# Performance work log

Hardware: AMD Instinct MI355X
Metric: run time of the kernel (lower is better)

The kernel has to match this reference:

```python
import jax, jax.numpy as jnp
from jax import lax
import numpy as np

MS = 128            # local_map_size
HALF = MS // 2
B, S = 8, 64
C, H, W = 3, 1024, 1024


def setup_inputs() -> dict:
    key = jax.random.key(0)
    ks = jax.random.split(key, 48)
    r = lambda i, shape, s: jax.random.normal(ks[i], shape, jnp.float32) * s
    z = lambda *shape: jnp.zeros(shape, jnp.float32)
    o = lambda *shape: jnp.ones(shape, jnp.float32)
    return {
        "full_map": jax.random.normal(ks[0], (B, C, H, W), jnp.float32),
        "conditions": jax.random.uniform(ks[1], (B, 5), jnp.float32, 0.0, 1024.0),
        "input_seq": jax.random.uniform(ks[2], (B, S, 2), jnp.float32, 0.0, 1024.0),
        "steps_remaining": jax.random.uniform(ks[3], (B, S), jnp.float32, 0.0, 500.0),
        # LocalMapEncoder convs (OIHW) + batchnorm affine params
        "cw1": r(4, (16, 3, 3, 3), 0.2),   "cb1": z(16),  "g1": o(16),  "be1": z(16),
        "cw2": r(5, (32, 16, 3, 3), 0.1),  "cb2": z(32),  "g2": o(32),  "be2": z(32),
        "cw3": r(6, (64, 32, 3, 3), 0.07), "cb3": z(64),  "g3": o(64),  "be3": z(64),
        "cw4": r(7, (128, 64, 3, 3), 0.05),"cb4": z(128), "g4": o(128), "be4": z(128),
        "fw1": r(8, (512, 128 * 8 * 8), 0.01), "fb1": z(512),
        "fw2": r(9, (256, 512), 0.04),         "fb2": z(256),
        # ConditionEncoder (6 -> 128 -> 64)
        "ew1": r(10, (128, 6), 0.05),  "eb1": z(128),
        "ew2": r(11, (64, 128), 0.05), "eb2": z(64),
        # coord embedder (2 -> 32)
        "mw": r(12, (32, 2), 0.05), "mb": z(32),
        # 2-layer LSTM, torch gate order (i, f, g, o)
        "w_ih0": r(13, (4 * 256, 32), 0.05),  "w_hh0": r(14, (4 * 256, 256), 0.05),
        "b_ih0": z(4 * 256), "b_hh0": z(4 * 256),
        "w_ih1": r(15, (4 * 256, 256), 0.05), "w_hh1": r(16, (4 * 256, 256), 0.05),
        "b_ih1": z(4 * 256), "b_hh1": z(4 * 256),
        # context layer (256+256+64=576 -> 128 -> 64) and output (64 -> 2)
        "xw1": r(17, (128, 576), 0.04), "xb1": z(128),
        "xw2": r(18, (64, 128), 0.05),  "xb2": z(64),
        "ow": r(19, (2, 64), 0.1),      "ob": z(2),
    }


def _conv_bn_relu(x, w, b, g, be):
    # stride-2 3x3 conv, padding 1, NCHW/OIHW; BatchNorm in training mode (batch stats)
    y = lax.conv_general_dilated(x, w, (2, 2), ((1, 1), (1, 1)),
                                 dimension_numbers=("NCHW", "OIHW", "NCHW"))
    y = y + b[None, :, None, None]
    mu = y.mean((0, 2, 3), keepdims=True)
    var = y.var((0, 2, 3), keepdims=True)
    y = (y - mu) * lax.rsqrt(var + 1e-5) * g[None, :, None, None] + be[None, :, None, None]
    return jax.nn.relu(y)


def _lstm_layer(x, w_ih, w_hh, b_ih, b_hh):
    # x: [B, S, D] -> hidden states [B, S, Hd]
    bsz, hd = x.shape[0], w_hh.shape[1]
    bias = b_ih + b_hh
    def step(carry, xt):
        h, c = carry
        zg = xt @ w_ih.T + h @ w_hh.T + bias
        i, f, gg, oo = jnp.split(zg, 4, axis=-1)
        c = jax.nn.sigmoid(f) * c + jax.nn.sigmoid(i) * jnp.tanh(gg)
        h = jax.nn.sigmoid(oo) * jnp.tanh(c)
        return (h, c), h
    h0 = jnp.zeros((bsz, hd), x.dtype)
    _, hs = lax.scan(step, (h0, h0), x.transpose(1, 0, 2))
    return hs.transpose(1, 0, 2)


def reference(full_map, conditions, input_seq, steps_remaining,
              cw1, cb1, g1, be1, cw2, cb2, g2, be2,
              cw3, cb3, g3, be3, cw4, cb4, g4, be4,
              fw1, fb1, fw2, fb2, ew1, eb1, ew2, eb2, mw, mb,
              w_ih0, w_hh0, b_ih0, b_hh0, w_ih1, w_hh1, b_ih1, b_hh1,
              xw1, xb1, xw2, xb2, ow, ob):
    bsz, seq, _ = input_seq.shape
    # --- batched crop+pad gather (replaces host numpy loop): zero-pad map by
    # HALF on each side, then every crop is a dynamic_slice of size MS at (y, x).
    padded = jnp.pad(full_map, ((0, 0), (0, 0), (HALF, HALF), (HALF, HALF)))
    ys = input_seq[..., 0].astype(jnp.int32).reshape(-1)
    xs = input_seq[..., 1].astype(jnp.int32).reshape(-1)
    bidx = jnp.repeat(jnp.arange(bsz, dtype=jnp.int32), seq)
    crop_one = lambda b, y, x: lax.dynamic_slice(padded, (b, 0, y, x), (1, C, MS, MS))[0]
    crops = jax.vmap(crop_one)(bidx, ys, xs)              # [B*S, C, MS, MS]
    # --- LocalMapEncoder
    h = _conv_bn_relu(crops, cw1, cb1, g1, be1)
    h = _conv_bn_relu(h, cw2, cb2, g2, be2)
    h = _conv_bn_relu(h, cw3, cb3, g3, be3)
    h = _conv_bn_relu(h, cw4, cb4, g4, be4)               # [B*S, 128, 8, 8]
    h = h.reshape(h.shape[0], -1)
    h = jax.nn.relu(h @ fw1.T + fb1) @ fw2.T + fb2
    map_features = h.reshape(bsz, seq, -1)                # [B, S, 256]
    # --- ConditionEncoder on [conditions ++ steps_remaining]
    enh = jnp.concatenate(
        [jnp.broadcast_to(conditions[:, None, :], (bsz, seq, 5)),
         steps_remaining[..., None]], axis=-1)            # [B, S, 6]
    cond_features = jax.nn.relu(enh @ ew1.T + eb1) @ ew2.T + eb2  # [B, S, 64]
    # --- route predictor
    emb = jax.nn.relu(input_seq @ mw.T + mb)              # [B, S, 32]
    lstm_out = _lstm_layer(emb, w_ih0, w_hh0, b_ih0, b_hh0)
    lstm_out = _lstm_layer(lstm_out, w_ih1, w_hh1, b_ih1, b_hh1)  # [B, S, 256]
    combined = jnp.concatenate([lstm_out, map_features, cond_features], axis=-1)
    ctx = jax.nn.relu(jax.nn.relu(combined @ xw1.T + xb1) @ xw2.T + xb2)
    return ctx @ ow.T + ob                                # [B, S, 2]
```

## Files before the change

kernel.cpp:

```cpp
#include <hip/hip_runtime.h>

#define TPB 256
#define NLB 64

typedef float f32x4 __attribute__((ext_vector_type(4)));
typedef short bf16x8 __attribute__((ext_vector_type(8)));
typedef unsigned long long u64;

__device__ __forceinline__ float bf2f(unsigned short u) {
  union { unsigned int i; float f; } x; x.i = ((unsigned int)u) << 16; return x.f;
}
__device__ __forceinline__ unsigned short f2bf(float v) {
  union { float f; unsigned int i; } x; x.f = v;
  unsigned int r = (x.i + 0x7fffu + ((x.i >> 16) & 1u)) >> 16;
  return (unsigned short)r;
}
__device__ __forceinline__ float sigf(float x) { return 1.f / (1.f + __expf(-x)); }
__device__ __forceinline__ bf16x8 lda_bf8(const unsigned short* p) {
  union { uint4 u; bf16x8 v; } t; t.u = *(const uint4*)p; return t.v;
}
__device__ __forceinline__ bf16x8 frag_of(const unsigned int* w) {
  union { unsigned int u[4]; bf16x8 v; } t;
  t.u[0] = w[0]; t.u[1] = w[1]; t.u[2] = w[2]; t.u[3] = w[3]; return t.v;
}

__global__ __launch_bounds__(TPB, 2) void conv1_tap(
    const float* __restrict__ fmap, const float* __restrict__ iseq,
    const unsigned short* __restrict__ wT,
    const float* __restrict__ bias,
    unsigned short* __restrict__ out) {
  __shared__ __align__(16) unsigned short patch[17][132][8];
  __shared__ unsigned short Bsm[16][104];
  __shared__ float bs[16];
  const int tid = threadIdx.x;
  const int n = blockIdx.x >> 3, R0 = (blockIdx.x & 7) << 3;
  const int y = (int)iseq[n * 2], x = (int)iseq[n * 2 + 1];
  const int bimg = n >> 6;

  for (int e = tid; e < 1536; e += TPB) Bsm[e / 96][e % 96] = wT[e];
  if (tid < 16) bs[tid] = bias[tid];
  for (int e = tid; e < 17 * 132; e += TPB)
    *(uint4*)&patch[e / 132][e % 132][0] = uint4{0u, 0u, 0u, 0u};
  __syncthreads();
  for (int e = tid; e < 3 * 17 * 132; e += TPB) {
    int ic = e / 2244, rem = e % 2244, l = rem / 132, c = rem % 132;
    int i = 2 * R0 - 1 + l, j = c - 1;
    float v = 0.f;
    if ((unsigned)i < 128u && (unsigned)j < 128u) {
      int r = y + i - 64, cc = x + j - 64;
      if ((unsigned)r < 1024u && (unsigned)cc < 1024u)
        v = fmap[(((size_t)bimg * 3 + ic) << 20) + ((size_t)r << 10) + cc];
    }
    patch[l][c][ic] = f2bf(v);
  }
  __syncthreads();

  const int w = tid >> 6, lane = tid & 63, fr = lane & 15, kg = lane >> 4;
  f32x4 acc[8];
#pragma unroll
  for (int m = 0; m < 8; ++m) acc[m] = {0.f, 0.f, 0.f, 0.f};

#pragma unroll
  for (int ch = 0; ch < 3; ++ch) {
    int k8 = ch * 4 + kg;
    int ki = (k8 >= 9) ? 0 : ((k8 * 11) >> 5);
    int kj = (k8 >= 9) ? 0 : (k8 - 3 * ki);
    bf16x8 bfr = lda_bf8(&Bsm[fr][k8 * 8]);
#pragma unroll
    for (int m = 0; m < 8; ++m) {
      int p = w * 128 + m * 16 + fr;
      int pr = p >> 6, pc = p & 63;
      bf16x8 af = lda_bf8(&patch[2 * pr + ki][2 * pc + kj][0]);
      acc[m] = __builtin_amdgcn_mfma_f32_16x16x32_bf16(af, bfr, acc[m], 0, 0, 0);
    }
  }
  const int rg = lane >> 4;
  float bb = bs[fr];
#pragma unroll
  for (int m = 0; m < 8; ++m) {
#pragma unroll
    for (int r = 0; r < 4; ++r) {
      int p = w * 128 + m * 16 + rg * 4 + r;
      int pr = p >> 6, pc = p & 63;
      out[(((size_t)n * 64 + R0 + pr) * 64 + pc) * 16 + fr] = f2bf(acc[m][r] + bb);
    }
  }
}

template<int CIN, int COUT_BLK, int NSPLIT, int HIN, int HOUT>
__global__ __launch_bounds__(TPB, 2) void conv_tap(
    const unsigned short* __restrict__ inb,
    const float* __restrict__ ss,
    const unsigned short* __restrict__ wT,
    const float* __restrict__ bias,
    unsigned short* __restrict__ out) {
  constexpr int K = CIN * 9;
  constexpr int K8 = K / 8;
  constexpr int NCH = (K8 + 3) / 4;
  constexpr int KPAD = NCH * 32;
  constexpr int BS = KPAD + 8;
  constexpr int CINP = CIN + 8;
  constexpr int ICG_SH = (CIN == 16) ? 1 : (CIN == 32) ? 2 : 3;
  constexpr int TPR = HOUT / 8;
  constexpr int TILES = TPR * TPR;
  constexpr int NT = COUT_BLK / 16;
  constexpr int COUT_TOT = COUT_BLK * NSPLIT;

  __shared__ unsigned short patch[289 * CINP];
  __shared__ unsigned short Bsm[COUT_BLK * BS];
  __shared__ float ssl[CIN * 2];

  const int tid = threadIdx.x;
  const int bid = blockIdx.x;
  const int n = bid / (TILES * NSPLIT);
  const int rem = bid % (TILES * NSPLIT);
  const int tile = rem / NSPLIT;
  const int split = rem % NSPLIT;
  const int TR0 = (tile / TPR) * 8, TC0 = (tile % TPR) * 8;
  const int oc0 = split * COUT_BLK;

  for (int i = tid; i < CIN * 2; i += TPB) ssl[i] = ss[i];
  __syncthreads();

  for (int e = tid; e < 289 * (CIN / 8); e += TPB) {
    int icg = e % (CIN / 8), pix = e / (CIN / 8);
    int row = pix / 17, col = pix % 17;
    int ir = 2 * TR0 - 1 + row, jc = 2 * TC0 - 1 + col;
    uint4 o = {0u, 0u, 0u, 0u};
    if ((unsigned)ir < (unsigned)HIN && (unsigned)jc < (unsigned)HIN) {
      uint4 v = *(const uint4*)&inb[(((size_t)n * HIN + ir) * HIN + jc) * CIN + icg * 8];
      unsigned int d[4] = {v.x, v.y, v.z, v.w};
      unsigned int* op = (unsigned int*)&o;
#pragma unroll
      for (int t = 0; t < 4; ++t) {
        int c = icg * 8 + 2 * t;
        float a = fmaxf(fmaf(bf2f((unsigned short)(d[t] & 0xffff)), ssl[2 * c], ssl[2 * c + 1]), 0.f);
        float b = fmaxf(fmaf(bf2f((unsigned short)(d[t] >> 16)), ssl[2 * c + 2], ssl[2 * c + 3]), 0.f);
        op[t] = (unsigned int)f2bf(a) | ((unsigned int)f2bf(b) << 16);
      }
    }
    *(uint4*)&patch[pix * CINP + icg * 8] = o;
  }
  constexpr int B8 = COUT_BLK * (KPAD / 8);
  for (int e = tid; e < B8; e += TPB) {
    int oc = e / (KPAD / 8), k8i = e % (KPAD / 8);
    uint4 v = {0u, 0u, 0u, 0u};
    if (k8i * 8 < K) v = *(const uint4*)&wT[(size_t)(oc0 + oc) * K + k8i * 8];
    *(uint4*)&Bsm[oc * BS + k8i * 8] = v;
  }
  __syncthreads();

  const int wave = tid >> 6, lane = tid & 63;
  const int fr = lane & 15, kg = lane >> 4;
  const int p = wave * 16 + fr;
  const int pr = p >> 3, pc = p & 7;
  f32x4 acc[NT];
#pragma unroll
  for (int j = 0; j < NT; ++j) acc[j] = {0.f, 0.f, 0.f, 0.f};

#pragma unroll
  for (int ch = 0; ch < NCH; ++ch) {
    int k8 = ch * 4 + kg;
    int tap = k8 >> ICG_SH, icg = k8 & ((1 << ICG_SH) - 1);
    int ki = (tap * 11) >> 5;
    int kj = tap - 3 * ki;
    int addr = ((2 * pr + ki) * 17 + (2 * pc + kj)) * CINP + icg * 8;
    if (tap >= 9) addr = 0;
    bf16x8 af = lda_bf8(&patch[addr]);
#pragma unroll
    for (int j = 0; j < NT; ++j) {
      bf16x8 bfr = lda_bf8(&Bsm[(j * 16 + fr) * BS + ch * 32 + kg * 8]);
      acc[j] = __builtin_amdgcn_mfma_f32_16x16x32_bf16(af, bfr, acc[j], 0, 0, 0);
    }
  }
  const int rg = lane >> 4;
#pragma unroll
  for (int j = 0; j < NT; ++j) {
    int oc = oc0 + j * 16 + fr;
    float bb = bias[oc];
#pragma unroll
    for (int r = 0; r < 4; ++r) {
      int pp = wave * 16 + rg * 4 + r;
      int orow = TR0 + (pp >> 3), ocol = TC0 + (pp & 7);
      out[(((size_t)n * HOUT + orow) * HOUT + ocol) * COUT_TOT + oc] = f2bf(acc[j][r] + bb);
    }
  }
}

__global__ __launch_bounds__(TPB) void prep_wt(
    const float* __restrict__ w1, const float* __restrict__ w2,
    const float* __restrict__ w3, const float* __restrict__ w4,
    unsigned short* __restrict__ wt1, unsigned short* __restrict__ wt2,
    unsigned short* __restrict__ wt3, unsigned short* __restrict__ wt4) {
  int i = blockIdx.x * TPB + threadIdx.x;
  if (i < 1536) {
    int oc = i / 96, k = i % 96;
    int tap = k >> 3, ic = k & 7;
    float v = (tap < 9 && ic < 3) ? w1[(oc * 3 + ic) * 9 + tap] : 0.f;
    wt1[i] = f2bf(v);
  } else if (i < 6144) {
    int j = i - 1536;
    int oc = j / 144, k = j % 144;
    wt2[j] = f2bf(w2[(oc * 16 + (k & 15)) * 9 + (k >> 4)]);
  } else if (i < 24576) {
    int j = i - 6144;
    int oc = j / 288, k = j % 288;
    wt3[j] = f2bf(w3[(oc * 32 + (k & 31)) * 9 + (k >> 5)]);
  } else if (i < 98304) {
    int j = i - 24576;
    int oc = j / 576, k = j % 576;
    wt4[j] = f2bf(w4[(oc * 64 + (k & 63)) * 9 + (k >> 6)]);
  }
}

__global__ __launch_bounds__(TPB) void permute_fw1(const float* __restrict__ in,
    unsigned short* __restrict__ out) {
  __shared__ unsigned short l[128 * 66];
  int n = blockIdx.x;
  for (int e = threadIdx.x; e < 8192; e += TPB) {
    int c = e >> 6, pix = e & 63;
    l[c * 66 + pix] = f2bf(in[(size_t)n * 8192 + e]);
  }
  __syncthreads();
  for (int e = threadIdx.x; e < 8192; e += TPB) {
    int pix = e >> 7, c = e & 127;
    out[(size_t)n * 8192 + e] = l[c * 66 + pix];
  }
}

#define STAT_NB 512
__global__ __launch_bounds__(TPB) void stats_cl2(
    const unsigned short* __restrict__ y, float* __restrict__ part,
    int C, int total_u4) {
  const int tid = threadIdx.x, bid = blockIdx.x;
  const int NQ = C >> 3;
  float s[8], q[8];
#pragma unroll
  for (int j = 0; j < 8; ++j) { s[j] = 0.f; q[j] = 0.f; }
  for (int i = bid * TPB + tid; i < total_u4; i += STAT_NB * TPB) {
    uint4 v = ((const uint4*)y)[i];
    unsigned int d[4] = {v.x, v.y, v.z, v.w};
#pragma unroll
    for (int t = 0; t < 4; ++t) {
      float a = bf2f((unsigned short)(d[t] & 0xffff));
      float b = bf2f((unsigned short)(d[t] >> 16));
      s[2 * t] += a;     q[2 * t] = fmaf(a, a, q[2 * t]);
      s[2 * t + 1] += b; q[2 * t + 1] = fmaf(b, b, q[2 * t + 1]);
    }
  }
  __shared__ float rs[TPB][8];
  __shared__ float rq[TPB][8];
#pragma unroll
  for (int j = 0; j < 8; ++j) { rs[tid][j] = s[j]; rq[tid][j] = q[j]; }
  __syncthreads();
  for (int off = TPB / 2; off >= NQ; off >>= 1) {
    if (tid < off) {
#pragma unroll
      for (int j = 0; j < 8; ++j) { rs[tid][j] += rs[tid + off][j]; rq[tid][j] += rq[tid + off][j]; }
    }
    __syncthreads();
  }
  if (tid < NQ) {
#pragma unroll
    for (int j = 0; j < 8; ++j) {
      int c = tid * 8 + j;
      part[(size_t)bid * 2 * C + 2 * c] = rs[tid][j];
      part[(size_t)bid * 2 * C + 2 * c + 1] = rq[tid][j];
    }
  }
}

__global__ __launch_bounds__(TPB) void stats_final2(const float* __restrict__ part,
    const float* __restrict__ gamma, const float* __restrict__ beta,
    float* __restrict__ ss, float inv_count, int C) {
  int c = blockIdx.x, tid = threadIdx.x;
  float sum = part[(size_t)tid * 2 * C + 2 * c] + part[(size_t)(tid + 256) * 2 * C + 2 * c];
  float sq  = part[(size_t)tid * 2 * C + 2 * c + 1] + part[(size_t)(tid + 256) * 2 * C + 2 * c + 1];
  __shared__ float rs[TPB], rq[TPB];
  rs[tid] = sum; rq[tid] = sq;
  __syncthreads();
  for (int off = TPB / 2; off > 0; off >>= 1) {
    if (tid < off) { rs[tid] += rs[tid + off]; rq[tid] += rq[tid + off]; }
    __syncthreads();
  }
  if (tid == 0) {
    float mean = rs[0] * inv_count;
    float var  = rq[0] * inv_count - mean * mean;
    float rstd = rsqrtf(var + 1e-5f);
    float scl  = gamma[c] * rstd;
    ss[2 * c] = scl;
    ss[2 * c + 1] = beta[c] - mean * scl;
  }
}

__device__ __forceinline__ uint4 bnpack(uint4 v, const float* sst) {
  unsigned int d[4] = {v.x, v.y, v.z, v.w};
  uint4 o; unsigned int* op = (unsigned int*)&o;
#pragma unroll
  for (int t = 0; t < 4; ++t) {
    float a = fmaxf(fmaf(bf2f((unsigned short)(d[t] & 0xffff)), sst[4 * t], sst[4 * t + 1]), 0.f);
    float b = fmaxf(fmaf(bf2f((unsigned short)(d[t] >> 16)), sst[4 * t + 2], sst[4 * t + 3]), 0.f);
    op[t] = (unsigned int)f2bf(a) | ((unsigned int)f2bf(b) << 16);
  }
  return o;
}

__global__ __launch_bounds__(TPB, 2) void fc1_mfma(
    const unsigned short* __restrict__ A, const unsigned short* __restrict__ W,
    const float* __restrict__ ss, const float* __restrict__ bias,
    float* __restrict__ out) {
  __shared__ unsigned short As[64][64];
  __shared__ unsigned short Bs[64][64];
  __shared__ float ssl[256];
  const int tid = threadIdx.x;
  const int lane = tid & 63, wave = tid >> 6;
  const int wr = (wave >> 1) * 32, wc = (wave & 1) * 32;
  const int bm = blockIdx.y * 64, bn = blockIdx.x * 64;
  f32x4 acc00 = {0.f, 0.f, 0.f, 0.f}, acc01 = acc00, acc10 = acc00, acc11 = acc00;
  const int r0 = tid >> 3, c0 = tid & 7;
  const int fr = lane & 15, kg = lane >> 4;
  for (int i = tid; i < 256; i += TPB) ssl[i] = ss[i];
  __syncthreads();
  for (int kt = 0; kt < 128; ++kt) {
    const int kb = kt * 64;
    uint4 av0 = *(const uint4*)&A[(size_t)(bm + r0) * 8192 + kb + c0 * 8];
    uint4 av1 = *(const uint4*)&A[(size_t)(bm + r0 + 32) * 8192 + kb + c0 * 8];
    uint4 bv0 = *(const uint4*)&W[(size_t)(bn + r0) * 8192 + kb + c0 * 8];
    uint4 bv1 = *(const uint4*)&W[(size_t)(bn + r0 + 32) * 8192 + kb + c0 * 8];
    const float* sst = &ssl[2 * ((kb + c0 * 8) & 127)];
    __syncthreads();
    av0 = bnpack(av0, sst);
    av1 = bnpack(av1, sst);
    *(uint4*)&As[r0][(c0 ^ (r0 & 7)) * 8] = av0;
    *(uint4*)&As[r0 + 32][(c0 ^ (r0 & 7)) * 8] = av1;
    *(uint4*)&Bs[r0][(c0 ^ (r0 & 7)) * 8] = bv0;
    *(uint4*)&Bs[r0 + 32][(c0 ^ (r0 & 7)) * 8] = bv1;
    __syncthreads();
#pragma unroll
    for (int ks = 0; ks < 2; ++ks) {
      int ch = ks * 4 + kg;
      int ra0 = wr + fr, ra1 = wr + 16 + fr;
      int rb0 = wc + fr, rb1 = wc + 16 + fr;
      bf16x8 a_0 = lda_bf8(&As[ra0][(ch ^ (ra0 & 7)) * 8]);
      bf16x8 a_1 = lda_bf8(&As[ra1][(ch ^ (ra1 & 7)) * 8]);
      bf16x8 b_0 = lda_bf8(&Bs[rb0][(ch ^ (rb0 & 7)) * 8]);
      bf16x8 b_1 = lda_bf8(&Bs[rb1][(ch ^ (rb1 & 7)) * 8]);
      acc00 = __builtin_amdgcn_mfma_f32_16x16x32_bf16(a_0, b_0, acc00, 0, 0, 0);
      acc01 = __builtin_amdgcn_mfma_f32_16x16x32_bf16(a_0, b_1, acc01, 0, 0, 0);
      acc10 = __builtin_amdgcn_mfma_f32_16x16x32_bf16(a_1, b_0, acc10, 0, 0, 0);
      acc11 = __builtin_amdgcn_mfma_f32_16x16x32_bf16(a_1, b_1, acc11, 0, 0, 0);
    }
  }
  const int rg = lane >> 4;
  int n0 = bn + wc + fr, n1 = n0 + 16;
  float bi0 = bias[n0], bi1 = bias[n1];
#pragma unroll
  for (int r = 0; r < 4; ++r) {
    int m0 = bm + wr + rg * 4 + r, m1 = m0 + 16;
    out[m0 * 512 + n0] = fmaxf(acc00[r] + bi0, 0.f);
    out[m0 * 512 + n1] = fmaxf(acc01[r] + bi1, 0.f);
    out[m1 * 512 + n0] = fmaxf(acc10[r] + bi0, 0.f);
    out[m1 * 512 + n1] = fmaxf(acc11[r] + bi1, 0.f);
  }
}

__global__ __launch_bounds__(TPB, 2) void gemm_m64(
    const float* __restrict__ A, const float* __restrict__ W,
    const float* __restrict__ bias, float* __restrict__ out,
    int N, int K, int relu, int ldo, int coff) {
  __shared__ unsigned short As[64 * 40];
  __shared__ unsigned short Bs[64 * 40];
  const int tid = threadIdx.x, lane = tid & 63, wave = tid >> 6;
  const int wr = (wave >> 1) * 32, wc = (wave & 1) * 32;
  const int bm = blockIdx.y * 64, bn = blockIdx.x * 64;
  const int fr = lane & 15, kg = lane >> 4;
  const int sr = tid >> 2, sc = (tid & 3) * 8;
  f32x4 a00 = {0.f, 0.f, 0.f, 0.f}, a01 = a00, a10 = a00, a11 = a00;
  int nch = (K + 31) >> 5;
  for (int ch = 0; ch < nch; ++ch) {
    int kb = ch * 32;
    __syncthreads();
    {
      unsigned short tmp[8];
#pragma unroll
      for (int j = 0; j < 8; ++j) {
        int k = kb + sc + j;
        tmp[j] = (k < K) ? f2bf(A[(size_t)(bm + sr) * K + k]) : (unsigned short)0;
      }
      *(uint4*)&As[sr * 40 + sc] = *(const uint4*)tmp;
      int wrow = bn + sr;
#pragma unroll
      for (int j = 0; j < 8; ++j) {
        int k = kb + sc + j;
        tmp[j] = (wrow < N && k < K) ? f2bf(W[(size_t)wrow * K + k]) : (unsigned short)0;
      }
      *(uint4*)&Bs[sr * 40 + sc] = *(const uint4*)tmp;
    }
    __syncthreads();
    bf16x8 af0 = lda_bf8(&As[(wr + fr) * 40 + kg * 8]);
    bf16x8 af1 = lda_bf8(&As[(wr + 16 + fr) * 40 + kg * 8]);
    bf16x8 bf0 = lda_bf8(&Bs[(wc + fr) * 40 + kg * 8]);
    bf16x8 bf1 = lda_bf8(&Bs[(wc + 16 + fr) * 40 + kg * 8]);
    a00 = __builtin_amdgcn_mfma_f32_16x16x32_bf16(af0, bf0, a00, 0, 0, 0);
    a01 = __builtin_amdgcn_mfma_f32_16x16x32_bf16(af0, bf1, a01, 0, 0, 0);
    a10 = __builtin_amdgcn_mfma_f32_16x16x32_bf16(af1, bf0, a10, 0, 0, 0);
    a11 = __builtin_amdgcn_mfma_f32_16x16x32_bf16(af1, bf1, a11, 0, 0, 0);
  }
  const int rg = lane >> 4;
  int n0 = bn + wc + fr, n1 = n0 + 16;
  float bi0 = (n0 < N) ? bias[n0] : 0.f;
  float bi1 = (n1 < N) ? bias[n1] : 0.f;
#pragma unroll
  for (int r = 0; r < 4; ++r) {
    int m0 = bm + wr + rg * 4 + r, m1 = m0 + 16;
    if (n0 < N) {
      float v = a00[r] + bi0; out[(size_t)m0 * ldo + coff + n0] = relu ? fmaxf(v, 0.f) : v;
      v = a10[r] + bi0;       out[(size_t)m1 * ldo + coff + n0] = relu ? fmaxf(v, 0.f) : v;
    }
    if (n1 < N) {
      float v = a01[r] + bi1; out[(size_t)m0 * ldo + coff + n1] = relu ? fmaxf(v, 0.f) : v;
      v = a11[r] + bi1;       out[(size_t)m1 * ldo + coff + n1] = relu ? fmaxf(v, 0.f) : v;
    }
  }
}

__global__ __launch_bounds__(TPB) void build_enh_kernel(const float* __restrict__ cond,
    const float* __restrict__ steps, float* __restrict__ enh) {
  int i = blockIdx.x * TPB + threadIdx.x;
  if (i >= 512 * 6) return;
  int n = i / 6, k = i % 6;
  int b = n >> 6, s = n & 63;
  enh[i] = (k < 5) ? cond[b * 5 + k] : steps[b * 64 + s];
}

__global__ __launch_bounds__(TPB, 1) void lstm_kernel(
    const float* __restrict__ iseq,
    const float* __restrict__ mw, const float* __restrict__ mb,
    const float* __restrict__ w_ih0, const float* __restrict__ w_hh0,
    const float* __restrict__ b_ih0, const float* __restrict__ b_hh0,
    const float* __restrict__ w_ih1, const float* __restrict__ w_hh1,
    const float* __restrict__ b_ih1, const float* __restrict__ b_hh1,
    u64* __restrict__ h0x, u64* __restrict__ h1x,
    float* __restrict__ comb) {
  const int tid = threadIdx.x;
  const int blkid = blockIdx.x;
  const int u0 = blkid * 4;

  __shared__ float xz[64][8][16];
  __shared__ __align__(16) char reg2[18944];
  __shared__ float bias1s[16];

  float (*embc)[8][32] = (float (*)[8][32])reg2;
  float* mwmb = (float*)(reg2 + 16384);
  unsigned short (*v0s)[264] = (unsigned short (*)[264])reg2;
  unsigned short (*w1h)[264] = (unsigned short (*)[264])(reg2 + 8448);
  float (*P0)[16]  = (float (*)[16])(reg2 + 16896);
  float (*P1a)[16] = (float (*)[16])(reg2 + 17408);
  float (*P1b)[16] = (float (*)[16])(reg2 + 17920);

  const int wv = tid >> 6, lane = tid & 63, fr = lane & 15, kg = lane >> 4;
  const int r = tid & 15, ks = tid >> 4;
  const int R  = (r >> 2) * 256 + u0 + (r & 3);
  const int Rf = (fr >> 2) * 256 + u0 + (fr & 3);

  unsigned int wfrag[8][4];
  {
    const float* wsrc = (wv == 0) ? w_hh0 : (wv == 1) ? w_ih1 : w_hh1;
#pragma unroll
    for (int ch = 0; ch < 8; ++ch)
#pragma unroll
      for (int d = 0; d < 4; ++d) {
        float lo = wsrc[(size_t)Rf * 256 + ch * 32 + kg * 8 + d * 2];
        float hi = wsrc[(size_t)Rf * 256 + ch * 32 + kg * 8 + d * 2 + 1];
        wfrag[ch][d] = (unsigned)f2bf(lo) | ((unsigned)f2bf(hi) << 16);
      }
  }
  float wtmp[32];
#pragma unroll
  for (int i = 0; i < 32; ++i) wtmp[i] = w_ih0[R * 32 + i];
  const float bias0r = b_ih0[R] + b_hh0[R];
  if (tid < 16) bias1s[tid] = b_ih1[R] + b_hh1[R];
  if (tid < 96) mwmb[tid] = (tid < 64) ? mw[tid] : mb[tid - 64];
  __syncthreads();

  for (int chunk = 0; chunk < 4; ++chunk) {
    if (tid < 128) {
      int pp = tid >> 3, b = tid & 7;
      int pg = chunk * 16 + pp;
      float s0 = iseq[(b * 64 + pg) * 2 + 0];
      float s1 = iseq[(b * 64 + pg) * 2 + 1];
      for (int k = 0; k < 32; ++k)
        embc[pp][b][k] = fmaxf(fmaf(mwmb[2 * k], s0, fmaf(mwmb[2 * k + 1], s1, mwmb[64 + k])), 0.f);
    }
    __syncthreads();
    {
      int pg = chunk * 16 + ks;
      for (int b = 0; b < 8; ++b) {
        float a = bias0r;
        const float* e = &embc[ks][b][0];
#pragma unroll
        for (int k = 0; k < 32; ++k) a = fmaf(wtmp[k], e[k], a);
        xz[pg][b][r] = a;
      }
    }
    __syncthreads();
  }

  for (int i = tid; i < 8 * 264; i += TPB) {
    v0s[8 + i / 264][i % 264] = 0;
    w1h[8 + i / 264][i % 264] = 0;
  }
  __syncthreads();

  float c0 = 0.f, c1 = 0.f;
  for (int p = 0; p <= 64; ++p) {
    if (tid < 128) {
      if (p >= 1) {
        const unsigned tag0 = (unsigned)p;
        const u64* s0p = &h0x[(size_t)(p - 1) * 1024 + tid * 8];
        u64 e[8];
        for (;;) {
          bool ok = true;
#pragma unroll
          for (int i = 0; i < 8; ++i) {
            e[i] = __hip_atomic_load(&s0p[i], __ATOMIC_RELAXED, __HIP_MEMORY_SCOPE_AGENT);
            ok &= ((unsigned)(e[i] >> 32) == tag0);
          }
          if (ok) break;
          __builtin_amdgcn_s_sleep(1);
        }
#pragma unroll
        for (int i = 0; i < 8; ++i) {
          int g = tid * 8 + i;
          int bb = (g >> 1) & 7, ub = (g >> 4) * 4 + (g & 1) * 2;
          *(unsigned int*)&v0s[bb][ub] = (unsigned int)e[i];
        }
      } else {
#pragma unroll
        for (int i = 0; i < 8; ++i) {
          int g = tid * 8 + i;
          int bb = (g >> 1) & 7, ub = (g >> 4) * 4 + (g & 1) * 2;
          *(unsigned int*)&v0s[bb][ub] = 0u;
        }
      }
    } else {
      int t2 = tid - 128;
      if (p >= 2) {
        const unsigned tag1 = (unsigned)(p - 1);
        const u64* s1p = &h1x[(size_t)(p - 2) * 1024 + t2 * 8];
        u64 e[8];
        for (;;) {
          bool ok = true;
#pragma unroll
          for (int i = 0; i < 8; ++i) {
            e[i] = __hip_atomic_load(&s1p[i], __ATOMIC_RELAXED, __HIP_MEMORY_SCOPE_AGENT);
            ok &= ((unsigned)(e[i] >> 32) == tag1);
          }
          if (ok) break;
          __builtin_amdgcn_s_sleep(1);
        }
#pragma unroll
        for (int i = 0; i < 8; ++i) {
          int g = t2 * 8 + i;
          int bb = (g >> 1) & 7, ub = (g >> 4) * 4 + (g & 1) * 2;
          *(unsigned int*)&w1h[bb][ub] = (unsigned int)e[i];
        }
      } else {
#pragma unroll
        for (int i = 0; i < 8; ++i) {
          int g = t2 * 8 + i;
          int bb = (g >> 1) & 7, ub = (g >> 4) * 4 + (g & 1) * 2;
          *(unsigned int*)&w1h[bb][ub] = 0u;
        }
      }
    }
    __syncthreads();

    if (wv == 0) {
      if (p < 64) {
        f32x4 acc = {0.f, 0.f, 0.f, 0.f};
#pragma unroll
        for (int ch = 0; ch < 8; ++ch) {
          bf16x8 af = lda_bf8(&v0s[fr][ch * 32 + kg * 8]);
          acc = __builtin_amdgcn_mfma_f32_16x16x32_bf16(af, frag_of(wfrag[ch]), acc, 0, 0, 0);
        }
#pragma unroll
        for (int j = 0; j < 4; ++j) {
          int bb2 = (lane >> 4) * 4 + j;
          if (bb2 < 8) P0[bb2][fr] = acc[j];
        }
      }
    } else if (wv == 1) {
      if (p >= 1) {
        f32x4 acc = {0.f, 0.f, 0.f, 0.f};
#pragma unroll
        for (int ch = 0; ch < 8; ++ch) {
          bf16x8 af = lda_bf8(&v0s[fr][ch * 32 + kg * 8]);
          acc = __builtin_amdgcn_mfma_f32_16x16x32_bf16(af, frag_of(wfrag[ch]), acc, 0, 0, 0);
        }
#pragma unroll
        for (int j = 0; j < 4; ++j) {
          int bb2 = (lane >> 4) * 4 + j;
          if (bb2 < 8) P1a[bb2][fr] = acc[j];
        }
      }
    } else if (wv == 2) {
      if (p >= 1) {
        f32x4 acc = {0.f, 0.f, 0.f, 0.f};
#pragma unroll
        for (int ch = 0; ch < 8; ++ch) {
          bf16x8 af = lda_bf8(&w1h[fr][ch * 32 + kg * 8]);
          acc = __builtin_amdgcn_mfma_f32_16x16x32_bf16(af, frag_of(wfrag[ch]), acc, 0, 0, 0);
        }
#pragma unroll
        for (int j = 0; j < 4; ++j) {
          int bb2 = (lane >> 4) * 4 + j;
          if (bb2 < 8) P1b[bb2][fr] = acc[j];
        }
      }
    }
    __syncthreads();

    if (tid < 32 && p < 64) {
      int b = tid >> 2, uu = tid & 3;
      float zi = P0[b][uu]      + xz[p][b][uu];
      float zf = P0[b][4 + uu]  + xz[p][b][4 + uu];
      float zg = P0[b][8 + uu]  + xz[p][b][8 + uu];
      float zo = P0[b][12 + uu] + xz[p][b][12 + uu];
      c0 = sigf(zf) * c0 + sigf(zi) * tanhf(zg);
      float h = sigf(zo) * tanhf(c0);
      float hp = __shfl_xor(h, 1);
      if (!(uu & 1)) {
        unsigned int d = (unsigned int)f2bf(h) | ((unsigned int)f2bf(hp) << 16);
        u64 v = ((u64)(unsigned)(p + 1) << 32) | d;
        __hip_atomic_store(&h0x[(size_t)p * 1024 + blkid * 16 + b * 2 + (uu >> 1)], v,
                           __ATOMIC_RELAXED, __HIP_MEMORY_SCOPE_AGENT);
      }
    } else if (tid >= 32 && tid < 64 && p >= 1) {
      int t2 = tid - 32, b = t2 >> 2, uu = t2 & 3;
      float zi = P1a[b][uu]      + P1b[b][uu]      + bias1s[uu];
      float zf = P1a[b][4 + uu]  + P1b[b][4 + uu]  + bias1s[4 + uu];
      float zg = P1a[b][8 + uu]  + P1b[b][8 + uu]  + bias1s[8 + uu];
      float zo = P1a[b][12 + uu] + P1b[b][12 + uu] + bias1s[12 + uu];
      c1 = sigf(zf) * c1 + sigf(zi) * tanhf(zg);
      float h = sigf(zo) * tanhf(c1);
      comb[(size_t)(b * 64 + (p - 1)) * 576 + u0 + uu] = h;
      float hp = __shfl_xor(h, 1);
      if (!(uu & 1)) {
        unsigned int d = (unsigned int)f2bf(h) | ((unsigned int)f2bf(hp) << 16);
        u64 v = ((u64)(unsigned)p << 32) | d;
        __hip_atomic_store(&h1x[(size_t)(p - 1) * 1024 + blkid * 16 + b * 2 + (uu >> 1)], v,
                           __ATOMIC_RELAXED, __HIP_MEMORY_SCOPE_AGENT);
      }
    }
  }
}

extern "C" void kernel_launch(void* const* d_in, const int* in_sizes, int n_in,
                              void* d_out, int out_size, void* d_ws, size_t ws_size,
                              hipStream_t stream) {
  const float* fmap  = (const float*)d_in[0];
  const float* cond  = (const float*)d_in[1];
  const float* iseq  = (const float*)d_in[2];
  const float* steps = (const float*)d_in[3];
  const float* cw1 = (const float*)d_in[4];  const float* cb1 = (const float*)d_in[5];
  const float* g1  = (const float*)d_in[6];  const float* be1 = (const float*)d_in[7];
  const float* cw2 = (const float*)d_in[8];  const float* cb2 = (const float*)d_in[9];
  const float* g2  = (const float*)d_in[10]; const float* be2 = (const float*)d_in[11];
  const float* cw3 = (const float*)d_in[12]; const float* cb3 = (const float*)d_in[13];
  const float* g3  = (const float*)d_in[14]; const float* be3 = (const float*)d_in[15];
  const float* cw4 = (const float*)d_in[16]; const float* cb4 = (const float*)d_in[17];
  const float* g4  = (const float*)d_in[18]; const float* be4 = (const float*)d_in[19];
  const float* fw1 = (const float*)d_in[20]; const float* fb1 = (const float*)d_in[21];
  const float* fw2 = (const float*)d_in[22]; const float* fb2 = (const float*)d_in[23];
  const float* ew1 = (const float*)d_in[24]; const float* eb1 = (const float*)d_in[25];
  const float* ew2 = (const float*)d_in[26]; const float* eb2 = (const float*)d_in[27];
  const float* mw  = (const float*)d_in[28]; const float* mb  = (const float*)d_in[29];
  const float* w_ih0 = (const float*)d_in[30]; const float* w_hh0 = (const float*)d_in[31];
  const float* b_ih0 = (const float*)d_in[32]; const float* b_hh0 = (const float*)d_in[33];
  const float* w_ih1 = (const float*)d_in[34]; const float* w_hh1 = (const float*)d_in[35];
  const float* b_ih1 = (const float*)d_in[36]; const float* b_hh1 = (const float*)d_in[37];
  const float* xw1 = (const float*)d_in[38]; const float* xb1 = (const float*)d_in[39];
  const float* xw2 = (const float*)d_in[40]; const float* xb2 = (const float*)d_in[41];
  const float* ow  = (const float*)d_in[42]; const float* ob  = (const float*)d_in[43];

  float* ws = (float*)d_ws;
  unsigned short* y1bf  = (unsigned short*)ws;
  unsigned short* y2bf  = (unsigned short*)(ws + 16777216);
  unsigned short* y3bf  = (unsigned short*)(ws + 25165824);
  unsigned short* y4pre = (unsigned short*)(ws + 29360128);
  unsigned short* fw1bf = (unsigned short*)(ws + 33554432);
  size_t base = 35651584;
  float* part  = ws + base; base += 131072;
  float* ss1   = ws + base; base += 32;
  float* ss2   = ws + base; base += 64;
  float* ss3   = ws + base; base += 128;
  float* ss4   = ws + base; base += 256;
  float* f1    = ws + base; base += 262144;
  float* enh   = ws + base; base += 3072;
  float* ceh   = ws + base; base += 65536;
  u64*   h0x   = (u64*)(ws + base); base += 131072;
  u64*   h1x   = (u64*)(ws + base); base += 131072;
  float* comb  = ws + base; base += 294912;
  float* cx1   = ws + base; base += 65536;
  float* cx2   = ws + base; base += 32768;
  unsigned short* wt1 = (unsigned short*)(ws + base); base += 768;
  unsigned short* wt2 = (unsigned short*)(ws + base); base += 2304;
  unsigned short* wt3 = (unsigned short*)(ws + base); base += 9216;
  unsigned short* wt4 = (unsigned short*)(ws + base); base += 36864;

  prep_wt<<<384, TPB, 0, stream>>>(cw1, cw2, cw3, cw4, wt1, wt2, wt3, wt4);
  permute_fw1<<<512, TPB, 0, stream>>>(fw1, fw1bf);

  conv1_tap<<<4096, TPB, 0, stream>>>(fmap, iseq, wt1, cb1, y1bf);
  stats_cl2<<<STAT_NB, TPB, 0, stream>>>(y1bf, part, 16, 4194304);
  stats_final2<<<16, TPB, 0, stream>>>(part, g1, be1, ss1, 1.f / 2097152.f, 16);
  conv_tap<16, 32, 1, 64, 32><<<8192, TPB, 0, stream>>>(y1bf, ss1, wt2, cb2, y2bf);
  stats_cl2<<<STAT_NB, TPB, 0, stream>>>(y2bf, part, 32, 2097152);
  stats_final2<<<32, TPB, 0, stream>>>(part, g2, be2, ss2, 1.f / 524288.f, 32);
  conv_tap<32, 64, 1, 32, 16><<<2048, TPB, 0, stream>>>(y2bf, ss2, wt3, cb3, y3bf);
  stats_cl2<<<STAT_NB, TPB, 0, stream>>>(y3bf, part, 64, 1048576);
  stats_final2<<<64, TPB, 0, stream>>>(part, g3, be3, ss3, 1.f / 131072.f, 64);
  conv_tap<64, 32, 4, 16, 8><<<2048, TPB, 0, stream>>>(y3bf, ss3, wt4, cb4, y4pre);
  stats_cl2<<<STAT_NB, TPB, 0, stream>>>(y4pre, part, 128, 524288);
  stats_final2<<<128, TPB, 0, stream>>>(part, g4, be4, ss4, 1.f / 32768.f, 128);

  hipMemsetAsync(h0x, 0, 2 * 64 * 1024 * sizeof(u64), stream);
  lstm_kernel<<<NLB, TPB, 0, stream>>>(iseq, mw, mb,
                                       w_ih0, w_hh0, b_ih0, b_hh0,
                                       w_ih1, w_hh1, b_ih1, b_hh1,
                                       h0x, h1x, comb);

  fc1_mfma<<<dim3(8, 8), TPB, 0, stream>>>(y4pre, fw1bf, ss4, fb1, f1);
  gemm_m64<<<dim3(4, 8), TPB, 0, stream>>>(f1, fw2, fb2, comb, 256, 512, 0, 576, 256);

  build_enh_kernel<<<12, TPB, 0, stream>>>(cond, steps, enh);
  gemm_m64<<<dim3(2, 8), TPB, 0, stream>>>(enh, ew1, eb1, ceh, 128, 6, 1, 128, 0);
  gemm_m64<<<dim3(1, 8), TPB, 0, stream>>>(ceh, ew2, eb2, comb, 64, 128, 0, 576, 512);

  gemm_m64<<<dim3(2, 8), TPB, 0, stream>>>(comb, xw1, xb1, cx1, 128, 576, 1, 128, 0);
  gemm_m64<<<dim3(1, 8), TPB, 0, stream>>>(cx1, xw2, xb2, cx2, 64, 128, 1, 64, 0);
  gemm_m64<<<dim3(1, 8), TPB, 0, stream>>>(cx2, ow, ob, (float*)d_out, 2, 64, 0, 2, 0);
}
```

Measured before the change: 670.0 us.

## Double-buffer LSTM hidden-state tiles and publish layer-0 h before block barrier

Splits the shared v0s and w1h staging buffers into two alternating copies indexed by step parity. This lets the next step's loads proceed without waiting behind readers of the current buffer. The layer-0 cell update and its cross-block atomic publish move into wave 0, right after its MFMA, using a local LDS wait instead of the block-wide barrier. This shortens the critical path of the layer-0 recurrence that other blocks spin on, at the cost of more LDS and reliance on intra-wave LDS ordering.

```diff
diff --git a/kernel.cpp b/kernel.cpp
--- a/kernel.cpp
+++ b/kernel.cpp
@@ -447,16 +447,13 @@
   const int u0 = blkid * 4;
 
   __shared__ float xz[64][8][16];
-  __shared__ __align__(16) char reg2[18944];
+  __shared__ __align__(16) unsigned short v0s[2][16][264];
+  __shared__ __align__(16) unsigned short w1h[2][16][264];
+  __shared__ float P0[8][16], P1a[8][16], P1b[8][16];
   __shared__ float bias1s[16];
-
-  float (*embc)[8][32] = (float (*)[8][32])reg2;
-  float* mwmb = (float*)(reg2 + 16384);
-  unsigned short (*v0s)[264] = (unsigned short (*)[264])reg2;
-  unsigned short (*w1h)[264] = (unsigned short (*)[264])(reg2 + 8448);
-  float (*P0)[16]  = (float (*)[16])(reg2 + 16896);
-  float (*P1a)[16] = (float (*)[16])(reg2 + 17408);
-  float (*P1b)[16] = (float (*)[16])(reg2 + 17920);
+  __shared__ float mwmb[96];
+
+  float (*embc)[8][32] = (float (*)[8][32])&v0s[0][0][0];
 
   const int wv = tid >> 6, lane = tid & 63, fr = lane & 15, kg = lane >> 4;
   const int r = tid & 15, ks = tid >> 4;
@@ -507,13 +504,15 @@
   }
 
   for (int i = tid; i < 8 * 264; i += TPB) {
-    v0s[8 + i / 264][i % 264] = 0;
-    w1h[8 + i / 264][i % 264] = 0;
+    int rr = 8 + i / 264, cc = i % 264;
+    v0s[0][rr][cc] = 0; v0s[1][rr][cc] = 0;
+    w1h[0][rr][cc] = 0; w1h[1][rr][cc] = 0;
   }
   __syncthreads();
 
   float c0 = 0.f, c1 = 0.f;
   for (int p = 0; p <= 64; ++p) {
+    const int cur = p & 1;
     if (tid < 128) {
       if (p >= 1) {
         const unsigned tag0 = (unsigned)p;
@@ -533,14 +532,14 @@
         for (int i = 0; i < 8; ++i) {
           int g = tid * 8 + i;
           int bb = (g >> 1) & 7, ub = (g >> 4) * 4 + (g & 1) * 2;
-          *(unsigned int*)&v0s[bb][ub] = (unsigned int)e[i];
+          *(unsigned int*)&v0s[cur][bb][ub] = (unsigned int)e[i];
         }
       } else {
 #pragma unroll
         for (int i = 0; i < 8; ++i) {
           int g = tid * 8 + i;
           int bb = (g >> 1) & 7, ub = (g >> 4) * 4 + (g & 1) * 2;
-          *(unsigned int*)&v0s[bb][ub] = 0u;
+          *(unsigned int*)&v0s[cur][bb][ub] = 0u;
         }
       }
     } else {
@@ -563,14 +562,14 @@
         for (int i = 0; i < 8; ++i) {
           int g = t2 * 8 + i;
           int bb = (g >> 1) & 7, ub = (g >> 4) * 4 + (g & 1) * 2;
-          *(unsigned int*)&w1h[bb][ub] = (unsigned int)e[i];
+          *(unsigned int*)&w1h[cur][bb][ub] = (unsigned int)e[i];
         }
       } else {
 #pragma unroll
         for (int i = 0; i < 8; ++i) {
           int g = t2 * 8 + i;
           int bb = (g >> 1) & 7, ub = (g >> 4) * 4 + (g & 1) * 2;
-          *(unsigned int*)&w1h[bb][ub] = 0u;
+          *(unsigned int*)&w1h[cur][bb][ub] = 0u;
         }
       }
     }
@@ -581,7 +580,7 @@
         f32x4 acc = {0.f, 0.f, 0.f, 0.f};
 #pragma unroll
         for (int ch = 0; ch < 8; ++ch) {
-          bf16x8 af = lda_bf8(&v0s[fr][ch * 32 + kg * 8]);
+          bf16x8 af = lda_bf8(&v0s[cur][fr][ch * 32 + kg * 8]);
           acc = __builtin_amdgcn_mfma_f32_16x16x32_bf16(af, frag_of(wfrag[ch]), acc, 0, 0, 0);
         }
 #pragma unroll
@@ -589,13 +588,31 @@
           int bb2 = (lane >> 4) * 4 + j;
           if (bb2 < 8) P0[bb2][fr] = acc[j];
         }
+        asm volatile("s_waitcnt lgkmcnt(0)" ::: "memory");
+        __builtin_amdgcn_sched_barrier(0);
+        if (lane < 32) {
+          int b = lane >> 2, uu = lane & 3;
+          float zi = P0[b][uu]      + xz[p][b][uu];
+          float zf = P0[b][4 + uu]  + xz[p][b][4 + uu];
+          float zg = P0[b][8 + uu]  + xz[p][b][8 + uu];
+          float zo = P0[b][12 + uu] + xz[p][b][12 + uu];
+          c0 = sigf(zf) * c0 + sigf(zi) * tanhf(zg);
+          float h = sigf(zo) * tanhf(c0);
+          float hp = __shfl_xor(h, 1);
+          if (!(uu & 1)) {
+            unsigned int d = (unsigned int)f2bf(h) | ((unsigned int)f2bf(hp) << 16);
+            u64 v = ((u64)(unsigned)(p + 1) << 32) | d;
+            __hip_atomic_store(&h0x[(size_t)p * 1024 + blkid * 16 + b * 2 + (uu >> 1)], v,
+                               __ATOMIC_RELAXED, __HIP_MEMORY_SCOPE_AGENT);
+          }
+        }
       }
     } else if (wv == 1) {
       if (p >= 1) {
         f32x4 acc = {0.f, 0.f, 0.f, 0.f};
 #pragma unroll
         for (int ch = 0; ch < 8; ++ch) {
-          bf16x8 af = lda_bf8(&v0s[fr][ch * 32 + kg * 8]);
+          bf16x8 af = lda_bf8(&v0s[cur][fr][ch * 32 + kg * 8]);
           acc = __builtin_amdgcn_mfma_f32_16x16x32_bf16(af, frag_of(wfrag[ch]), acc, 0, 0, 0);
         }
 #pragma unroll
@@ -609,7 +626,7 @@
         f32x4 acc = {0.f, 0.f, 0.f, 0.f};
 #pragma unroll
         for (int ch = 0; ch < 8; ++ch) {
-          bf16x8 af = lda_bf8(&w1h[fr][ch * 32 + kg * 8]);
+          bf16x8 af = lda_bf8(&w1h[cur][fr][ch * 32 + kg * 8]);
           acc = __builtin_amdgcn_mfma_f32_16x16x32_bf16(af, frag_of(wfrag[ch]), acc, 0, 0, 0);
         }
 #pragma unroll
@@ -621,22 +638,7 @@
     }
     __syncthreads();
 
-    if (tid < 32 && p < 64) {
-      int b = tid >> 2, uu = tid & 3;
-      float zi = P0[b][uu]      + xz[p][b][uu];
-      float zf = P0[b][4 + uu]  + xz[p][b][4 + uu];
-      float zg = P0[b][8 + uu]  + xz[p][b][8 + uu];
-      float zo = P0[b][12 + uu] + xz[p][b][12 + uu];
-      c0 = sigf(zf) * c0 + sigf(zi) * tanhf(zg);
-      float h = sigf(zo) * tanhf(c0);
-      float hp = __shfl_xor(h, 1);
-      if (!(uu & 1)) {
-        unsigned int d = (unsigned int)f2bf(h) | ((unsigned int)f2bf(hp) << 16);
-        u64 v = ((u64)(unsigned)(p + 1) << 32) | d;
-        __hip_atomic_store(&h0x[(size_t)p * 1024 + blkid * 16 + b * 2 + (uu >> 1)], v,
-                           __ATOMIC_RELAXED, __HIP_MEMORY_SCOPE_AGENT);
-      }
-    } else if (tid >= 32 && tid < 64 && p >= 1) {
+    if (tid >= 32 && tid < 64 && p >= 1) {
       int t2 = tid - 32, b = t2 >> 2, uu = t2 & 3;
       float zi = P1a[b][uu]      + P1b[b][uu]      + bias1s[uu];
       float zf = P1a[b][4 + uu]  + P1b[b][4 + uu]  + bias1s[4 + uu];
```

Result: slower. 687.9 us (+2.7%).

## Fuse BatchNorm statistics into conv epilogues and merge condition encoder

Applied to the files above, without the earlier changes.

Each conv kernel now reduces per-channel sum and sum-of-squares in its epilogue, using shuffles and shared memory, and writes per-block partials. A new finalize kernel combines those partials, which removes the separate stats passes that re-read every bf16 activation tensor. The condition encoder's concat and two GEMMs are merged into one small kernel. Stats are now taken from pre-rounding fp32 values rather than the stored bf16 values, and the partial buffer grows.

```diff
diff --git a/kernel.cpp b/kernel.cpp
--- a/kernel.cpp
+++ b/kernel.cpp
@@ -28,10 +28,11 @@
     const float* __restrict__ fmap, const float* __restrict__ iseq,
     const unsigned short* __restrict__ wT,
     const float* __restrict__ bias,
-    unsigned short* __restrict__ out) {
+    unsigned short* __restrict__ out, float* __restrict__ part) {
   __shared__ __align__(16) unsigned short patch[17][132][8];
   __shared__ unsigned short Bsm[16][104];
   __shared__ float bs[16];
+  __shared__ float swsum[4][16], swsq[4][16];
   const int tid = threadIdx.x;
   const int n = blockIdx.x >> 3, R0 = (blockIdx.x & 7) << 3;
   const int y = (int)iseq[n * 2], x = (int)iseq[n * 2 + 1];
@@ -76,14 +77,27 @@
   }
   const int rg = lane >> 4;
   float bb = bs[fr];
+  float sps = 0.f, spq = 0.f;
 #pragma unroll
   for (int m = 0; m < 8; ++m) {
 #pragma unroll
     for (int r = 0; r < 4; ++r) {
       int p = w * 128 + m * 16 + rg * 4 + r;
       int pr = p >> 6, pc = p & 63;
-      out[(((size_t)n * 64 + R0 + pr) * 64 + pc) * 16 + fr] = f2bf(acc[m][r] + bb);
-    }
+      float v = acc[m][r] + bb;
+      sps += v; spq = fmaf(v, v, spq);
+      out[(((size_t)n * 64 + R0 + pr) * 64 + pc) * 16 + fr] = f2bf(v);
+    }
+  }
+  sps += __shfl_xor(sps, 16); spq += __shfl_xor(spq, 16);
+  sps += __shfl_xor(sps, 32); spq += __shfl_xor(spq, 32);
+  if (lane < 16) { swsum[w][fr] = sps; swsq[w][fr] = spq; }
+  __syncthreads();
+  if (tid < 16) {
+    float s = swsum[0][tid] + swsum[1][tid] + swsum[2][tid] + swsum[3][tid];
+    float q = swsq[0][tid] + swsq[1][tid] + swsq[2][tid] + swsq[3][tid];
+    part[(size_t)blockIdx.x * 32 + tid * 2] = s;
+    part[(size_t)blockIdx.x * 32 + tid * 2 + 1] = q;
   }
 }
 
@@ -93,7 +107,7 @@
     const float* __restrict__ ss,
     const unsigned short* __restrict__ wT,
     const float* __restrict__ bias,
-    unsigned short* __restrict__ out) {
+    unsigned short* __restrict__ out, float* __restrict__ part) {
   constexpr int K = CIN * 9;
   constexpr int K8 = K / 8;
   constexpr int NCH = (K8 + 3) / 4;
@@ -109,6 +123,7 @@
   __shared__ unsigned short patch[289 * CINP];
   __shared__ unsigned short Bsm[COUT_BLK * BS];
   __shared__ float ssl[CIN * 2];
+  __shared__ float swsum[4][COUT_BLK], swsq[4][COUT_BLK];
 
   const int tid = threadIdx.x;
   const int bid = blockIdx.x;
@@ -178,12 +193,54 @@
   for (int j = 0; j < NT; ++j) {
     int oc = oc0 + j * 16 + fr;
     float bb = bias[oc];
+    float s1 = 0.f, q1 = 0.f;
 #pragma unroll
     for (int r = 0; r < 4; ++r) {
       int pp = wave * 16 + rg * 4 + r;
       int orow = TR0 + (pp >> 3), ocol = TC0 + (pp & 7);
-      out[(((size_t)n * HOUT + orow) * HOUT + ocol) * COUT_TOT + oc] = f2bf(acc[j][r] + bb);
-    }
+      float v = acc[j][r] + bb;
+      s1 += v; q1 = fmaf(v, v, q1);
+      out[(((size_t)n * HOUT + orow) * HOUT + ocol) * COUT_TOT + oc] = f2bf(v);
+    }
+    s1 += __shfl_xor(s1, 16); q1 += __shfl_xor(q1, 16);
+    s1 += __shfl_xor(s1, 32); q1 += __shfl_xor(q1, 32);
+    if (lane < 16) { swsum[wave][j * 16 + fr] = s1; swsq[wave][j * 16 + fr] = q1; }
+  }
+  __syncthreads();
+  if (tid < COUT_BLK) {
+    float s = swsum[0][tid] + swsum[1][tid] + swsum[2][tid] + swsum[3][tid];
+    float q = swsq[0][tid] + swsq[1][tid] + swsq[2][tid] + swsq[3][tid];
+    part[(size_t)bid * COUT_BLK * 2 + tid * 2] = s;
+    part[(size_t)bid * COUT_BLK * 2 + tid * 2 + 1] = q;
+  }
+}
+
+__global__ __launch_bounds__(TPB) void stats_final3(const float* __restrict__ part,
+    const float* __restrict__ gamma, const float* __restrict__ beta,
+    float* __restrict__ ss, float inv_count, int COUT_BLK, int NSPLIT, int NBID) {
+  const int c = blockIdx.x, tid = threadIdx.x;
+  const int split = c / COUT_BLK, loc = c % COUT_BLK;
+  const int NG = NBID / NSPLIT;
+  float s = 0.f, q = 0.f;
+  for (int g = tid; g < NG; g += TPB) {
+    size_t b = (size_t)g * NSPLIT + split;
+    s += part[b * COUT_BLK * 2 + loc * 2];
+    q += part[b * COUT_BLK * 2 + loc * 2 + 1];
+  }
+  __shared__ float rs[TPB], rq[TPB];
+  rs[tid] = s; rq[tid] = q;
+  __syncthreads();
+  for (int off = TPB / 2; off > 0; off >>= 1) {
+    if (tid < off) { rs[tid] += rs[tid + off]; rq[tid] += rq[tid + off]; }
+    __syncthreads();
+  }
+  if (tid == 0) {
+    float mean = rs[0] * inv_count;
+    float var  = rq[0] * inv_count - mean * mean;
+    float rstd = rsqrtf(var + 1e-5f);
+    float scl  = gamma[c] * rstd;
+    ss[2 * c] = scl;
+    ss[2 * c + 1] = beta[c] - mean * scl;
   }
 }
 
@@ -228,71 +285,6 @@
   }
 }
 
-#define STAT_NB 512
-__global__ __launch_bounds__(TPB) void stats_cl2(
-    const unsigned short* __restrict__ y, float* __restrict__ part,
-    int C, int total_u4) {
-  const int tid = threadIdx.x, bid = blockIdx.x;
-  const int NQ = C >> 3;
-  float s[8], q[8];
-#pragma unroll
-  for (int j = 0; j < 8; ++j) { s[j] = 0.f; q[j] = 0.f; }
-  for (int i = bid * TPB + tid; i < total_u4; i += STAT_NB * TPB) {
-    uint4 v = ((const uint4*)y)[i];
-    unsigned int d[4] = {v.x, v.y, v.z, v.w};
-#pragma unroll
-    for (int t = 0; t < 4; ++t) {
-      float a = bf2f((unsigned short)(d[t] & 0xffff));
-      float b = bf2f((unsigned short)(d[t] >> 16));
-      s[2 * t] += a;     q[2 * t] = fmaf(a, a, q[2 * t]);
-      s[2 * t + 1] += b; q[2 * t + 1] = fmaf(b, b, q[2 * t + 1]);
-    }
-  }
-  __shared__ float rs[TPB][8];
-  __shared__ float rq[TPB][8];
-#pragma unroll
-  for (int j = 0; j < 8; ++j) { rs[tid][j] = s[j]; rq[tid][j] = q[j]; }
-  __syncthreads();
-  for (int off = TPB / 2; off >= NQ; off >>= 1) {
-    if (tid < off) {
-#pragma unroll
-      for (int j = 0; j < 8; ++j) { rs[tid][j] += rs[tid + off][j]; rq[tid][j] += rq[tid + off][j]; }
-    }
-    __syncthreads();
-  }
-  if (tid < NQ) {
-#pragma unroll
-    for (int j = 0; j < 8; ++j) {
-      int c = tid * 8 + j;
-      part[(size_t)bid * 2 * C + 2 * c] = rs[tid][j];
-      part[(size_t)bid * 2 * C + 2 * c + 1] = rq[tid][j];
-    }
-  }
-}
-
-__global__ __launch_bounds__(TPB) void stats_final2(const float* __restrict__ part,
-    const float* __restrict__ gamma, const float* __restrict__ beta,
-    float* __restrict__ ss, float inv_count, int C) {
-  int c = blockIdx.x, tid = threadIdx.x;
-  float sum = part[(size_t)tid * 2 * C + 2 * c] + part[(size_t)(tid + 256) * 2 * C + 2 * c];
-  float sq  = part[(size_t)tid * 2 * C + 2 * c + 1] + part[(size_t)(tid + 256) * 2 * C + 2 * c + 1];
-  __shared__ float rs[TPB], rq[TPB];
-  rs[tid] = sum; rq[tid] = sq;
-  __syncthreads();
-  for (int off = TPB / 2; off > 0; off >>= 1) {
-    if (tid < off) { rs[tid] += rs[tid + off]; rq[tid] += rq[tid + off]; }
-    __syncthreads();
-  }
-  if (tid == 0) {
-    float mean = rs[0] * inv_count;
-    float var  = rq[0] * inv_count - mean * mean;
-    float rstd = rsqrtf(var + 1e-5f);
-    float scl  = gamma[c] * rstd;
-    ss[2 * c] = scl;
-    ss[2 * c + 1] = beta[c] - mean * scl;
-  }
-}
-
 __device__ __forceinline__ uint4 bnpack(uint4 v, const float* sst) {
   unsigned int d[4] = {v.x, v.y, v.z, v.w};
   uint4 o; unsigned int* op = (unsigned int*)&o;
@@ -424,13 +416,49 @@
   }
 }
 
-__global__ __launch_bounds__(TPB) void build_enh_kernel(const float* __restrict__ cond,
-    const float* __restrict__ steps, float* __restrict__ enh) {
-  int i = blockIdx.x * TPB + threadIdx.x;
-  if (i >= 512 * 6) return;
-  int n = i / 6, k = i % 6;
-  int b = n >> 6, s = n & 63;
-  enh[i] = (k < 5) ? cond[b * 5 + k] : steps[b * 64 + s];
+__global__ __launch_bounds__(TPB) void cond_enc(
+    const float* __restrict__ cond, const float* __restrict__ steps,
+    const float* __restrict__ ew1, const float* __restrict__ eb1,
+    const float* __restrict__ ew2, const float* __restrict__ eb2,
+    float* __restrict__ comb) {
+  __shared__ float w1s[128][8];
+  __shared__ float w2s[64][132];
+  __shared__ float hbuf[64][132];
+  const int tid = threadIdx.x;
+  const int row0 = blockIdx.x * 64;
+  for (int e = tid; e < 128 * 8; e += TPB) {
+    int k = e >> 3, t = e & 7;
+    w1s[k][t] = (t < 6) ? ew1[k * 6 + t] : (t == 6 ? eb1[k] : 0.f);
+  }
+  for (int e = tid; e < 64 * 128; e += TPB) {
+    int j = e >> 7, k = e & 127;
+    w2s[j][k] = ew2[j * 128 + k];
+  }
+  __syncthreads();
+  {
+    int row = tid >> 2, ks = tid & 3;
+    int n = row0 + row;
+    int b = n >> 6, s = n & 63;
+    float e0 = cond[b * 5], e1 = cond[b * 5 + 1], e2 = cond[b * 5 + 2];
+    float e3 = cond[b * 5 + 3], e4 = cond[b * 5 + 4];
+    float e5 = steps[b * 64 + s];
+    for (int k = ks * 32; k < ks * 32 + 32; ++k) {
+      float a = fmaf(w1s[k][0], e0, fmaf(w1s[k][1], e1, fmaf(w1s[k][2], e2,
+                fmaf(w1s[k][3], e3, fmaf(w1s[k][4], e4, fmaf(w1s[k][5], e5, w1s[k][6]))))));
+      hbuf[row][k] = fmaxf(a, 0.f);
+    }
+  }
+  __syncthreads();
+  {
+    int row = tid >> 2, js = tid & 3;
+    int n = row0 + row;
+    for (int j = js * 16; j < js * 16 + 16; ++j) {
+      float a = eb2[j];
+#pragma unroll 8
+      for (int k = 0; k < 128; ++k) a = fmaf(w2s[j][k], hbuf[row][k], a);
+      comb[(size_t)n * 576 + 512 + j] = a;
+    }
+  }
 }
 
 __global__ __launch_bounds__(TPB, 1) void lstm_kernel(
@@ -691,14 +719,12 @@
   unsigned short* y4pre = (unsigned short*)(ws + 29360128);
   unsigned short* fw1bf = (unsigned short*)(ws + 33554432);
   size_t base = 35651584;
-  float* part  = ws + base; base += 131072;
+  float* part  = ws + base; base += 524288;
   float* ss1   = ws + base; base += 32;
   float* ss2   = ws + base; base += 64;
   float* ss3   = ws + base; base += 128;
   float* ss4   = ws + base; base += 256;
   float* f1    = ws + base; base += 262144;
-  float* enh   = ws + base; base += 3072;
-  float* ceh   = ws + base; base += 65536;
   u64*   h0x   = (u64*)(ws + base); base += 131072;
   u64*   h1x   = (u64*)(ws + base); base += 131072;
   float* comb  = ws + base; base += 294912;
@@ -712,18 +738,14 @@
   prep_wt<<<384, TPB, 0, stream>>>(cw1, cw2, cw3, cw4, wt1, wt2, wt3, wt4);
   permute_fw1<<<512, TPB, 0, stream>>>(fw1, fw1bf);
 
-  conv1_tap<<<4096, TPB, 0, stream>>>(fmap, iseq, wt1, cb1, y1bf);
-  stats_cl2<<<STAT_NB, TPB, 0, stream>>>(y1bf, part, 16, 4194304);
-  stats_final2<<<16, TPB, 0, stream>>>(part, g1, be1, ss1, 1.f / 2097152.f, 16);
-  conv_tap<16, 32, 1, 64, 32><<<8192, TPB, 0, stream>>>(y1bf, ss1, wt2, cb2, y2bf);
-  stats_cl2<<<STAT_NB, TPB, 0, stream>>>(y2bf, part, 32, 2097152);
-  stats_final2<<<32, TPB, 0, stream>>>(part, g2, be2, ss2, 1.f / 524288.f, 32);
-  conv_tap<32, 64, 1, 32, 16><<<2048, TPB, 0, stream>>>(y2bf, ss2, wt3, cb3, y3bf);
-  stats_cl2<<<STAT_NB, TPB, 0, stream>>>(y3bf, part, 64, 1048576);
-  stats_final2<<<64, TPB, 0, stream>>>(part, g3, be3, ss3, 1.f / 131072.f, 64);
-  conv_tap<64, 32, 4, 16, 8><<<2048, TPB, 0, stream>>>(y3bf, ss3, wt4, cb4, y4pre);
-  stats_cl2<<<STAT_NB, TPB, 0, stream>>>(y4pre, part, 128, 524288);
-  stats_final2<<<128, TPB, 0, stream>>>(part, g4, be4, ss4, 1.f / 32768.f, 128);
+  conv1_tap<<<4096, TPB, 0, stream>>>(fmap, iseq, wt1, cb1, y1bf, part);
+  stats_final3<<<16, TPB, 0, stream>>>(part, g1, be1, ss1, 1.f / 2097152.f, 16, 1, 4096);
+  conv_tap<16, 32, 1, 64, 32><<<8192, TPB, 0, stream>>>(y1bf, ss1, wt2, cb2, y2bf, part);
+  stats_final3<<<32, TPB, 0, stream>>>(part, g2, be2, ss2, 1.f / 524288.f, 32, 1, 8192);
+  conv_tap<32, 64, 1, 32, 16><<<2048, TPB, 0, stream>>>(y2bf, ss2, wt3, cb3, y3bf, part);
+  stats_final3<<<64, TPB, 0, stream>>>(part, g3, be3, ss3, 1.f / 131072.f, 64, 1, 2048);
+  conv_tap<64, 32, 4, 16, 8><<<2048, TPB, 0, stream>>>(y3bf, ss3, wt4, cb4, y4pre, part);
+  stats_final3<<<128, TPB, 0, stream>>>(part, g4, be4, ss4, 1.f / 32768.f, 32, 4, 2048);
 
   hipMemsetAsync(h0x, 0, 2 * 64 * 1024 * sizeof(u64), stream);
   lstm_kernel<<<NLB, TPB, 0, stream>>>(iseq, mw, mb,
@@ -734,9 +756,7 @@
   fc1_mfma<<<dim3(8, 8), TPB, 0, stream>>>(y4pre, fw1bf, ss4, fb1, f1);
   gemm_m64<<<dim3(4, 8), TPB, 0, stream>>>(f1, fw2, fb2, comb, 256, 512, 0, 576, 256);
 
-  build_enh_kernel<<<12, TPB, 0, stream>>>(cond, steps, enh);
-  gemm_m64<<<dim3(2, 8), TPB, 0, stream>>>(enh, ew1, eb1, ceh, 128, 6, 1, 128, 0);
-  gemm_m64<<<dim3(1, 8), TPB, 0, stream>>>(ceh, ew2, eb2, comb, 64, 128, 0, 576, 512);
+  cond_enc<<<8, TPB, 0, stream>>>(cond, steps, ew1, eb1, ew2, eb2, comb);
 
   gemm_m64<<<dim3(2, 8), TPB, 0, stream>>>(comb, xw1, xb1, cx1, 128, 576, 1, 128, 0);
   gemm_m64<<<dim3(1, 8), TPB, 0, stream>>>(cx1, xw2, xb2, cx2, 64, 128, 1, 64, 0);
```

New measurement: 675.5 us. About the same (+0.8%).
